# Kernel optimization log

Hardware: AMD Instinct MI355X
Metric: run time of the kernel (lower is better)

Reference implementation:

```python
import jax, jax.numpy as jnp
import numpy as np
from jax import lax

RF = 19       # receptive field: layers*(kernel-1)+1 = 3*6+1
WINDOW = 12
N_MIX = 2
K = 20        # subgraph_size (top-k per row)
GDEP = 2
ALPHA = 0.05  # propalpha
EPS = 1e-5


def conv2d(x, w, b):
    # x: [N,C,H,W], w: [O,I,1,k], valid conv along time (last) axis
    o = lax.conv_general_dilated(x, w, (1, 1), 'VALID',
                                 dimension_numbers=('NCHW', 'OIHW', 'NCHW'))
    return o + b[None, :, None, None]


def dilated_inception(x, ws, b):
    # ws: kernels [co, ci, k] for k in (2,3,6,7); dilation factor is 1 here
    outs = [lax.conv_general_dilated(x, w[:, :, None, :], (1, 1), 'VALID',
                                     dimension_numbers=('NCHW', 'OIHW', 'NCHW'))
            for w in ws]
    L = outs[-1].shape[-1]  # truncate to shortest (largest kernel) length
    out = jnp.concatenate([o[..., -L:] for o in outs], axis=1)
    return out + b[None, :, None, None]


def build_adj(e1, e2, l1w, l1b, l2w, l2b):
    # e1,e2: [M2,N,D] embedding tables (idx = arange -> full table)
    # torch Linear: y = x @ W.T + b, W: [out,in]
    nv1 = jnp.einsum('mnd,mod->mno', e1, l1w) + l1b[:, None, :]
    nv2 = jnp.einsum('mnd,mod->mno', e2, l2w) + l2b[:, None, :]
    a = jnp.einsum('mnd,mkd->mnk', nv1, nv2)  # [M2, N, N] per-block adjacency
    rows = [jnp.concatenate([a[i * N_MIX + j] for j in range(N_MIX)], axis=1)
            for i in range(N_MIX)]
    adj = jnp.concatenate(rows, axis=0)  # [NT, NT]
    _, t = lax.top_k(adj, K)  # per-row top-k indices
    mask = jnp.zeros_like(adj).at[jnp.arange(adj.shape[0])[:, None], t].set(1.0)
    return adj * mask


def mixprop(x, adj, w, b):
    a = adj + jnp.eye(adj.shape[0], dtype=adj.dtype)
    a = a / jnp.sum(a, axis=1, keepdims=True)  # row-normalize
    h = x
    outs = [h]
    for _ in range(GDEP):
        h = ALPHA * x + (1.0 - ALPHA) * jnp.einsum('ncwl,vw->ncvl', h, a)
        outs.append(h)
    ho = jnp.concatenate(outs, axis=1)  # [B,(GDEP+1)*C,V,L]
    return jnp.einsum('ncvl,oc->novl', ho, w) + b[None, :, None, None]


def layernorm(x, w, b):
    # torch F.layer_norm over all dims except batch; idx = arange -> full affine
    mu = jnp.mean(x, axis=(1, 2, 3), keepdims=True)
    var = jnp.mean((x - mu) ** 2, axis=(1, 2, 3), keepdims=True)
    return (x - mu) * lax.rsqrt(var + EPS) * w[None] + b[None]


def setup_inputs() -> dict:
    keys = iter(jax.random.split(jax.random.key(0), 80))
    def rn(shape, s=0.1):
        return s * jax.random.normal(next(keys), shape, dtype=jnp.float32)
    d = {}
    d['x_in'] = jax.random.normal(next(keys), (32, 12, 500, 4), dtype=jnp.float32)
    d['start_w'] = rn((32, 1, 1, 1)); d['start_b'] = rn((32,))
    d['skip0_w'] = rn((64, 1, 1, 19)); d['skip0_b'] = rn((64,))
    d['emb1'] = rn((3, 4, 500, 40)); d['emb2'] = rn((3, 4, 500, 40))
    d['lin1_w'] = rn((3, 4, 40, 40)); d['lin1_b'] = rn((3, 4, 40))
    d['lin2_w'] = rn((3, 4, 40, 40)); d['lin2_b'] = rn((3, 4, 40))
    d['g1_w'] = rn((3, 32, 96)); d['g1_b'] = rn((3, 32))
    d['g2_w'] = rn((3, 32, 96)); d['g2_b'] = rn((3, 32))
    for pref in ('filt', 'gate'):
        for k in (2, 3, 6, 7):
            d[f'{pref}_w{k}'] = rn((3, 8, 32, k))
        d[f'{pref}_b'] = rn((3, 32))
    for i, L in zip((1, 2, 3), (13, 7, 1)):
        d[f'skip_w{i}'] = rn((64, 32, 1, L)); d[f'skip_b{i}'] = rn((64,))
        d[f'norm_w{i}'] = jnp.ones((32, 1000, L), jnp.float32)
        d[f'norm_b{i}'] = jnp.zeros((32, 1000, L), jnp.float32)
    d['skipE_w'] = rn((64, 32, 1, 1)); d['skipE_b'] = rn((64,))
    d['end1_w'] = rn((128, 64, 1, 1)); d['end1_b'] = rn((128,))
    d['end2_w'] = rn((12, 128, 1, 1)); d['end2_b'] = rn((12,))
    return d


def reference(x_in, start_w, start_b, skip0_w, skip0_b, emb1, emb2,
              lin1_w, lin1_b, lin2_w, lin2_b, g1_w, g1_b, g2_w, g2_b,
              filt_w2, filt_w3, filt_w6, filt_w7, filt_b,
              gate_w2, gate_w3, gate_w6, gate_w7, gate_b,
              skip_w1, skip_b1, skip_w2, skip_b2, skip_w3, skip_b3,
              norm_w1, norm_b1, norm_w2, norm_b2, norm_w3, norm_b3,
              skipE_w, skipE_b, end1_w, end1_b, end2_w, end2_b):
    feat = x_in[..., :-2]  # drop last 2 'time' features
    # split per-mode feature and stack along node dim: [B,T,2N,1]
    inp = jnp.concatenate([feat[..., 0:1], feat[..., 1:2]], axis=2)
    inp = jnp.transpose(inp, (0, 3, 2, 1))  # [B,1,2N,T]
    inp = jnp.pad(inp, ((0, 0), (0, 0), (0, 0), (RF - WINDOW, 0)))
    x = conv2d(inp, start_w, start_b)       # [B,32,1000,19]
    skip = conv2d(inp, skip0_w, skip0_b)    # [B,64,1000,1] (dropout=eval no-op)
    filt_ws = (filt_w2, filt_w3, filt_w6, filt_w7)
    gate_ws = (gate_w2, gate_w3, gate_w6, gate_w7)
    skips = ((skip_w1, skip_b1), (skip_w2, skip_b2), (skip_w3, skip_b3))
    norms = ((norm_w1, norm_b1), (norm_w2, norm_b2), (norm_w3, norm_b3))
    for i in range(3):
        adp = build_adj(emb1[i], emb2[i], lin1_w[i], lin1_b[i], lin2_w[i], lin2_b[i])
        residual = x
        x = mixprop(x, adp, g1_w[i], g1_b[i]) + mixprop(x, adp.T, g2_w[i], g2_b[i])
        f = jnp.tanh(dilated_inception(x, [w[i] for w in filt_ws], filt_b[i]))
        g = jax.nn.sigmoid(dilated_inception(x, [w[i] for w in gate_ws], gate_b[i]))
        x = f * g
        sw, sb = skips[i]
        skip = conv2d(x, sw, sb) + skip
        x = x + residual[..., -x.shape[3]:]
        nw, nb = norms[i]
        x = layernorm(x, nw, nb)
    skip = conv2d(x, skipE_w, skipE_b) + skip
    x = jax.nn.relu(skip)
    x = jax.nn.relu(conv2d(x, end1_w, end1_b))
    return conv2d(x, end2_w, end2_b)  # [B, horizon*out_dim0=12, 1000, 1]
```

## Files before the change

kernel.cpp:

```cpp
#include <hip/hip_runtime.h>
#include <math.h>


#define ALPHA_C 0.05f
#define EPS_C 1e-5f
#define NBC 32
#define CSCT_CAP 140000

__device__ float g_inp[32 * 19 * 1000];
__device__ float g_skip[32 * 64 * 1000];
__device__ __align__(16) float g_nv1[240000];
__device__ __align__(16) float g_nv2[240000];
__device__ __align__(16) int   g_tkcol[60000];
__device__ __align__(16) float g_tkval[60000];
__device__ float g_inv1[3000];
__device__ int   g_colcnt[3000];
__device__ float g_colsum[3000];
__device__ int   g_rp2[3 * 1001 + 1];
__device__ int   g_fill[3000];
__device__ int   g_cscr[60000];
__device__ float g_cscv[60000];
__device__ float g_inv2[3000];
__device__ float g_stats[3 * 64];
__device__ float g_nwT[672000];
__device__ float g_nbT[672000];
__device__ __align__(16) int2 g_pk1T[60000];
__device__ __align__(16) int2 g_cscT[3 * CSCT_CAP];
__device__ int   g_perm[3 * 1024];
__device__ int   g_degT[3 * 1024];
__device__ int   g_iperm[3 * 1000];
__device__ int   g_tOff[3 * 17];
__device__ float g_B0[(size_t)NBC * 32 * 19 * 1000];
__device__ float g_B1[(size_t)NBC * 32 * 19 * 1000];
__device__ float g_B2[(size_t)NBC * 32 * 19 * 1000];
__device__ float g_B3[(size_t)NBC * 32 * 19 * 1000];
__device__ float g_B4[(size_t)NBC * 32 * 19 * 1000];
__device__ float g_B5[(size_t)NBC * 32 * 19 * 1000];

__device__ __forceinline__ float* bufsel(int s)
{
    switch (s) {
        case 0: return g_B0;
        case 1: return g_B1;
        case 2: return g_B2;
        case 3: return g_B3;
        case 4: return g_B4;
        default: return g_B5;
    }
}

__global__ void k_init()
{
    int i = blockIdx.x * 256 + threadIdx.x;
    if (i < 3000) { g_colcnt[i] = 0; g_colsum[i] = 0.f; g_fill[i] = 0; }
    if (i < 192) g_stats[i] = 0.f;
}

__global__ void k_out_zero(float* __restrict__ out, int n)
{
    int i = blockIdx.x * 256 + threadIdx.x;
    if (i < n) out[i] = 0.0f;
}

__global__ void k_marker(float* __restrict__ out, float v)
{
    if (threadIdx.x == 0) out[0] = v;
}


__global__ void k_build_inp(const float* __restrict__ xin)
{
    int i = blockIdx.x * 256 + threadIdx.x;
    if (i >= 32 * 19 * 1000) return;
    int v = i % 1000;
    int t = (i / 1000) % 19;
    int b = i / 19000;
    float val = 0.f;
    if (t >= 7) {
        int tt = t - 7;
        int n = (v < 500) ? v : v - 500;
        int f = (v < 500) ? 0 : 1;
        val = xin[((b * 12 + tt) * 500 + n) * 4 + f];
    }
    g_inp[i] = val;
}

__global__ void k_packN(const float* __restrict__ nw0, const float* __restrict__ nb0,
                        const float* __restrict__ nw1, const float* __restrict__ nb1,
                        const float* __restrict__ nw2, const float* __restrict__ nb2)
{
    int i = blockIdx.x * 256 + threadIdx.x;
    if (i >= 672000) return;
    const float* nw;
    const float* nb;
    int L, e;
    if (i < 416000)      { nw = nw0; nb = nb0; L = 13; e = i; }
    else if (i < 640000) { nw = nw1; nb = nb1; L = 7;  e = i - 416000; }
    else                 { nw = nw2; nb = nb2; L = 1;  e = i - 640000; }
    int ch = e / 1000, v = e - ch * 1000;
    int c = ch / L, l = ch - c * L;
    int src = (c * 1000 + v) * L + l;
    g_nwT[i] = nw[src];
    g_nbT[i] = nb[src];
}

__global__ void k_nv(const float* __restrict__ e1, const float* __restrict__ e2,
                     const float* __restrict__ w1, const float* __restrict__ b1,
                     const float* __restrict__ w2, const float* __restrict__ b2)
{
    int i = blockIdx.x * 256 + threadIdx.x;
    if (i >= 12 * 500 * 40) return;
    int o = i % 40;
    int n = (i / 40) % 500;
    int m = i / (40 * 500);
    const float4* p1 = (const float4*)(e1 + (m * 500 + n) * 40);
    const float4* pw1 = (const float4*)(w1 + (m * 40 + o) * 40);
    const float4* p2 = (const float4*)(e2 + (m * 500 + n) * 40);
    const float4* pw2 = (const float4*)(w2 + (m * 40 + o) * 40);
    float a1 = b1[m * 40 + o], a2 = b2[m * 40 + o];
    for (int d = 0; d < 10; ++d) {
        float4 x1 = p1[d], y1 = pw1[d];
        float4 x2 = p2[d], y2 = pw2[d];
        a1 += x1.x * y1.x; a1 += x1.y * y1.y; a1 += x1.z * y1.z; a1 += x1.w * y1.w;
        a2 += x2.x * y2.x; a2 += x2.y * y2.y; a2 += x2.z * y2.z; a2 += x2.w * y2.w;
    }
    g_nv1[i] = a1;
    g_nv2[i] = a2;
}

__global__ __launch_bounds__(256) void k_adj_topk()
{
    __shared__ float wvv[4];
    __shared__ int wvi[4];
    __shared__ int wci;
    __shared__ int selc[20];
    __shared__ float selv[20];
    int li = blockIdx.x / 1000;
    int r = blockIdx.x % 1000;
    int tid = threadIdx.x;
    int wv = tid >> 6, lane = tid & 63;
    int bi = r / 500, n = r % 500;
    float rv0, rv1, rv2, rv3;
    {
        auto score = [&](int c) -> float {
            if (c >= 1000) return -INFINITY;
            int bj = c / 500, k = c % 500;
            int mg = li * 4 + 2 * bi + bj;
            const float4* a = (const float4*)(g_nv1 + (mg * 500 + n) * 40);
            const float4* b = (const float4*)(g_nv2 + (mg * 500 + k) * 40);
            float acc = 0.f;
#pragma unroll
            for (int d = 0; d < 10; ++d) {
                float4 av = a[d], bv = b[d];
                acc += av.x * bv.x; acc += av.y * bv.y;
                acc += av.z * bv.z; acc += av.w * bv.w;
            }
            return acc;
        };
        rv0 = score(tid);
        rv1 = score(tid + 256);
        rv2 = score(tid + 512);
        rv3 = score(tid + 768);
    }
    for (int sel = 0; sel < 20; ++sel) {
        float bv = rv0;
        int bidx = tid;
        if (rv1 > bv) { bv = rv1; bidx = tid + 256; }
        if (rv2 > bv) { bv = rv2; bidx = tid + 512; }
        if (rv3 > bv) { bv = rv3; bidx = tid + 768; }
#pragma unroll
        for (int m = 1; m < 64; m <<= 1) {
            float ov = __shfl_xor(bv, m);
            int oi = __shfl_xor(bidx, m);
            if (ov > bv || (ov == bv && oi < bidx)) { bv = ov; bidx = oi; }
        }
        if (lane == 0) { wvv[wv] = bv; wvi[wv] = bidx; }
        __syncthreads();
        if (tid == 0) {
            float fv = wvv[0];
            int fi = wvi[0];
#pragma unroll
            for (int k = 1; k < 4; ++k) {
                float ov = wvv[k];
                int oi = wvi[k];
                if (ov > fv || (ov == fv && oi < fi)) { fv = ov; fi = oi; }
            }
            int ci = fi;
            if (ci < 0 || ci > 999) ci = sel;
            selc[sel] = ci;
            selv[sel] = fv;
            g_tkcol[(li * 1000 + r) * 20 + sel] = ci;
            g_tkval[(li * 1000 + r) * 20 + sel] = fv;
            wci = ci;
        }
        __syncthreads();
        int ci = wci;
        if ((ci & 255) == tid) {
            int k = ci >> 8;
            if (k == 0) rv0 = -INFINITY;
            else if (k == 1) rv1 = -INFINITY;
            else if (k == 2) rv2 = -INFINITY;
            else rv3 = -INFINITY;
        }
    }
    if (tid < 20) {
        atomicAdd(&g_colcnt[li * 1000 + selc[tid]], 1);
        atomicAdd(&g_colsum[li * 1000 + selc[tid]], selv[tid]);
    }
    if (tid == 0) {
        float s = 0.f;
        for (int j = 0; j < 20; ++j) s += selv[j];
        g_inv1[li * 1000 + r] = 1.f / (s + 1.f);
    }
}

__global__ __launch_bounds__(256) void k_scanperm()
{
    __shared__ int s[1000];
    __shared__ int deg[1000];
    __shared__ int tmax[16];
    int li = blockIdx.x;
    int tid = threadIdx.x;
    for (int i = tid; i < 1000; i += 256) {
        int c = g_colcnt[li * 1000 + i];
        s[i] = c;
        deg[i] = c;
    }
    __syncthreads();
    if (tid == 0) {
        int run = 0;
        for (int i = 0; i < 1000; ++i) { int c = s[i]; s[i] = run; run += c; }
        g_rp2[li * 1001 + 1000] = run;
    }
    __syncthreads();
    for (int i = tid; i < 1000; i += 256) {
        g_rp2[li * 1001 + i] = s[i];
        g_inv2[li * 1000 + i] = 1.f / (g_colsum[li * 1000 + i] + 1.f);
    }
    for (int v = tid; v < 1000; v += 256) {
        int d = deg[v];
        int r = 0;
        for (int u = 0; u < 1000; ++u) {
            int du = deg[u];
            r += (du > d) || (du == d && u < v);
        }
        g_perm[li * 1024 + r] = v;
        g_degT[li * 1024 + r] = d;
        g_iperm[li * 1000 + v] = r;
        if ((r & 63) == 0) tmax[r >> 6] = d;
    }
    if (tid < 24) {
        g_perm[li * 1024 + 1000 + tid] = -1;
        g_degT[li * 1024 + 1000 + tid] = 0;
    }
    __syncthreads();
    if (tid == 0) {
        int off = 0;
        for (int t = 0; t < 16; ++t) {
            g_tOff[li * 17 + t] = off;
            off += 64 * tmax[t];
        }
        g_tOff[li * 17 + 16] = off;
    }
}

__global__ void k_scatter()
{
    int i = blockIdx.x * 256 + threadIdx.x;
    if (i >= 3 * 20000) return;
    int li = i / 20000;
    int e = i % 20000;
    int r = e / 20;
    int c = g_tkcol[i];
    if (c < 0) c = 0;
    if (c > 999) c = 999;
    float v = g_tkval[i];
    int pos = g_rp2[li * 1001 + c] + atomicAdd(&g_fill[li * 1000 + c], 1);
    if (pos < 0) pos = 0;
    if (pos > 19999) pos = 19999;
    g_cscr[li * 20000 + pos] = r;
    g_cscv[li * 20000 + pos] = v;
}

__global__ void k_packT1()
{
    int i = blockIdx.x * 256 + threadIdx.x;
    if (i >= 60000) return;
    int li = i / 20000;
    int e = i % 20000;
    int v = e / 20, j = e % 20;
    int c1 = g_tkcol[i];
    if (c1 < 0) c1 = 0;
    if (c1 > 999) c1 = 999;
    g_pk1T[li * 20000 + j * 1000 + v] = make_int2(c1 * 16, __float_as_int(g_tkval[i]));
}

__global__ void k_packT2()
{
    int i = blockIdx.x * 256 + threadIdx.x;
    if (i >= 3000) return;
    int li = i / 1000, v = i % 1000;
    int r = g_iperm[li * 1000 + v];
    int t = r >> 6, ln = r & 63;
    int j0 = g_rp2[li * 1001 + v];
    int d = g_rp2[li * 1001 + v + 1] - j0;
    int base = g_tOff[li * 17 + t];
    for (int j = 0; j < d; ++j) {
        int row = g_cscr[li * 20000 + j0 + j];
        if (row < 0) row = 0;
        if (row > 999) row = 999;
        int pos = base + j * 64 + ln;
        if (pos >= 0 && pos < CSCT_CAP)
            g_cscT[li * CSCT_CAP + pos] =
                make_int2(row * 16, __float_as_int(g_cscv[li * 20000 + j0 + j]));
    }
}


__global__ __launch_bounds__(256) void k_skip0(const float* __restrict__ w,
                                               const float* __restrict__ bb)
{
    __shared__ float s_inp[19 * 32];
    __shared__ float s_w[64 * 19];
    int b = blockIdx.y;
    int v0 = blockIdx.x * 32;
    int tid = threadIdx.x;
    for (int i = tid; i < 64 * 19; i += 256) s_w[i] = w[i];
    for (int i = tid; i < 19 * 32; i += 256) {
        int t = i / 32, vl = i % 32;
        int v = v0 + vl;
        s_inp[i] = (v < 1000) ? g_inp[(b * 19 + t) * 1000 + v] : 0.f;
    }
    __syncthreads();
    for (int e = tid; e < 64 * 32; e += 256) {
        int o = e / 32, vl = e % 32;
        int v = v0 + vl;
        if (v >= 1000) continue;
        float acc = bb[o];
#pragma unroll
        for (int t = 0; t < 19; ++t) acc += s_w[o * 19 + t] * s_inp[t * 32 + vl];
        g_skip[(b * 64 + o) * 1000 + v] = acc;
    }
}

__global__ __launch_bounds__(256, 5) void k_prop4(int xsel, int o1s, int o2s, int o3s, int o4s,
                                                  int li, int CH, int li0,
                                                  const float* __restrict__ sw,
                                                  const float* __restrict__ sb,
                                                  int noff)
{
    __shared__ float4 S[2000];
    const float* X = bufsel(xsel);
    float* o1 = bufsel(o1s);
    float* o2 = bufsel(o2s);
    float* o3 = bufsel(o3s);
    float* o4 = bufsel(o4s);
    const int2* pkT = g_pk1T + li * 20000;
    const int2* cT = g_cscT + (size_t)li * CSCT_CAP;
    const int* prm = g_perm + li * 1024;
    const int* dgT = g_degT + li * 1024;
    const int* tOf = g_tOff + li * 17;
    const float* iv1 = g_inv1 + li * 1000;
    const float* iv2 = g_inv2 + li * 1000;
    int n = blockIdx.y;
    int ch0 = blockIdx.x * 4;
    size_t gb = ((size_t)n * CH + ch0) * 1000;
    int tid = threadIdx.x;
    int wv = tid >> 6, lane = tid & 63;
    char* Ub = (char*)S;
    char* Wb = (char*)(S + 1000);
    float4* U4 = S;
    float4* W4 = S + 1000;

    auto csr_hop = [&](const char* sbuf, float4* dst, float* gout) {
        for (int it = 0; it < 4; ++it) {
            int v = it * 256 + tid;
            if (v >= 1000) break;
            const int2* mp = pkT + v;
            float4 a = *(const float4*)(sbuf + (size_t)v * 16);
#pragma unroll
            for (int jb = 0; jb < 5; ++jb) {
                int2 e0 = mp[(jb * 4 + 0) * 1000];
                int2 e1 = mp[(jb * 4 + 1) * 1000];
                int2 e2 = mp[(jb * 4 + 2) * 1000];
                int2 e3 = mp[(jb * 4 + 3) * 1000];
                float w0 = __int_as_float(e0.y), w1 = __int_as_float(e1.y);
                float w2 = __int_as_float(e2.y), w3 = __int_as_float(e3.y);
                float4 x0 = *(const float4*)(sbuf + e0.x);
                float4 x1 = *(const float4*)(sbuf + e1.x);
                float4 x2 = *(const float4*)(sbuf + e2.x);
                float4 x3 = *(const float4*)(sbuf + e3.x);
                a.x += w0 * x0.x + w1 * x1.x + w2 * x2.x + w3 * x3.x;
                a.y += w0 * x0.y + w1 * x1.y + w2 * x2.y + w3 * x3.y;
                a.z += w0 * x0.z + w1 * x1.z + w2 * x2.z + w3 * x3.z;
                a.w += w0 * x0.w + w1 * x1.w + w2 * x2.w + w3 * x3.w;
            }
            float s = iv1[v];
            a.x *= s; a.y *= s; a.z *= s; a.w *= s;
            if (dst) dst[v] = a;
            gout[gb + v] = a.x;
            gout[gb + 1000 + v] = a.y;
            gout[gb + 2000 + v] = a.z;
            gout[gb + 3000 + v] = a.w;
        }
    };

    auto csc_hop = [&](const char* sbuf, float4* dst) {
        for (int o = 0; o < 4; ++o) {
            int tile = o * 4 + ((o & 1) ? (3 - wv) : wv);
            int r = tile * 64 + lane;
            int v = prm[r];
            if (v < 0) continue;
            int d = dgT[r];
            const int2* mp = cT + tOf[tile] + lane;
            float4 a = *(const float4*)(sbuf + (size_t)v * 16);
            int j = 0;
            for (; j + 4 <= d; j += 4) {
                int2 e0 = mp[(j + 0) * 64];
                int2 e1 = mp[(j + 1) * 64];
                int2 e2 = mp[(j + 2) * 64];
                int2 e3 = mp[(j + 3) * 64];
                float w0 = __int_as_float(e0.y), w1 = __int_as_float(e1.y);
                float w2 = __int_as_float(e2.y), w3 = __int_as_float(e3.y);
                float4 x0 = *(const float4*)(sbuf + e0.x);
                float4 x1 = *(const float4*)(sbuf + e1.x);
                float4 x2 = *(const float4*)(sbuf + e2.x);
                float4 x3 = *(const float4*)(sbuf + e3.x);
                a.x += w0 * x0.x + w1 * x1.x + w2 * x2.x + w3 * x3.x;
                a.y += w0 * x0.y + w1 * x1.y + w2 * x2.y + w3 * x3.y;
                a.z += w0 * x0.z + w1 * x1.z + w2 * x2.z + w3 * x3.z;
                a.w += w0 * x0.w + w1 * x1.w + w2 * x2.w + w3 * x3.w;
            }
            for (; j < d; ++j) {
                int2 e = mp[j * 64];
                float w = __int_as_float(e.y);
                float4 x = *(const float4*)(sbuf + e.x);
                a.x += w * x.x; a.y += w * x.y; a.z += w * x.z; a.w += w * x.w;
            }
            float s = iv2[v];
            a.x *= s; a.y *= s; a.z *= s; a.w *= s;
            dst[v] = a;
        }
    };

    if (li0) {
        float swv0 = sw[(ch0 + 0) / 19], sbv0 = sb[(ch0 + 0) / 19];
        float swv1 = sw[(ch0 + 1) / 19], sbv1 = sb[(ch0 + 1) / 19];
        float swv2 = sw[(ch0 + 2) / 19], sbv2 = sb[(ch0 + 2) / 19];
        float swv3 = sw[(ch0 + 3) / 19], sbv3 = sb[(ch0 + 3) / 19];
        const float* i0 = g_inp + (n * 19 + (ch0 + 0) % 19) * 1000;
        const float* i1 = g_inp + (n * 19 + (ch0 + 1) % 19) * 1000;
        const float* i2 = g_inp + (n * 19 + (ch0 + 2) % 19) * 1000;
        const float* i3 = g_inp + (n * 19 + (ch0 + 3) % 19) * 1000;
        for (int it = 0; it < 4; ++it) {
            int v = it * 256 + tid;
            if (v >= 1000) break;
            float4 t;
            t.x = swv0 * i0[v] + sbv0;
            t.y = swv1 * i1[v] + sbv1;
            t.z = swv2 * i2[v] + sbv2;
            t.w = swv3 * i3[v] + sbv3;
            U4[v] = t;
        }
    } else {
        const float* pst = g_stats + (li - 1) * 64;
        float cnt = (float)CH * 1000.f;
        float mu = pst[n * 2] / cnt;
        float var = pst[n * 2 + 1] / cnt - mu * mu;
        float rs = rsqrtf(var + EPS_C);
        const float* nw0 = g_nwT + noff + (ch0 + 0) * 1000;
        const float* nw1 = g_nwT + noff + (ch0 + 1) * 1000;
        const float* nw2 = g_nwT + noff + (ch0 + 2) * 1000;
        const float* nw3 = g_nwT + noff + (ch0 + 3) * 1000;
        const float* nb0 = g_nbT + noff + (ch0 + 0) * 1000;
        const float* nb1 = g_nbT + noff + (ch0 + 1) * 1000;
        const float* nb2 = g_nbT + noff + (ch0 + 2) * 1000;
        const float* nb3 = g_nbT + noff + (ch0 + 3) * 1000;
        for (int it = 0; it < 4; ++it) {
            int v = it * 256 + tid;
            if (v >= 1000) break;
            float4 t;
            t.x = (X[gb + v] - mu) * rs * nw0[v] + nb0[v];
            t.y = (X[gb + 1000 + v] - mu) * rs * nw1[v] + nb1[v];
            t.z = (X[gb + 2000 + v] - mu) * rs * nw2[v] + nb2[v];
            t.w = (X[gb + 3000 + v] - mu) * rs * nw3[v] + nb3[v];
            U4[v] = t;
        }
    }
    __syncthreads();

    csr_hop(Ub, W4, o1);
    __syncthreads();

    csr_hop(Wb, (float4*)nullptr, o2);
    __syncthreads();

    csc_hop(Ub, W4);
    __syncthreads();

    for (int it = 0; it < 4; ++it) {
        int v = it * 256 + tid;
        if (v >= 1000) break;
        float4 t = W4[v];
        o3[gb + v] = t.x;
        o3[gb + 1000 + v] = t.y;
        o3[gb + 2000 + v] = t.z;
        o3[gb + 3000 + v] = t.w;
    }
    csc_hop(Wb, U4);
    __syncthreads();

    for (int it = 0; it < 4; ++it) {
        int v = it * 256 + tid;
        if (v >= 1000) break;
        float4 t = U4[v];
        o4[gb + v] = t.x;
        o4[gb + 1000 + v] = t.y;
        o4[gb + 2000 + v] = t.z;
        o4[gb + 3000 + v] = t.w;
    }
}

__global__ __launch_bounds__(256) void k_mix(int xs, int h1s, int h2s, int h3s, int h4s, int ms,
                                             const float* __restrict__ g1w, const float* __restrict__ g2w,
                                             const float* __restrict__ g1b, const float* __restrict__ g2b,
                                             int P, int li, int li0,
                                             const float* __restrict__ sw_,
                                             const float* __restrict__ sb_,
                                             int noff)
{
    __shared__ float sW[5 * 1024];
    __shared__ float sB[32];
    __shared__ float sWS[32];
    __shared__ float sSB[32];
    int tid = threadIdx.x;
    const float A = ALPHA_C, Bq = 1.f - ALPHA_C;
    for (int i = tid; i < 1024; i += 256) {
        int o = i >> 5, c = i & 31;
        float w1 = g1w[o * 96 + 32 + c], w2 = g1w[o * 96 + 64 + c];
        float w3 = g2w[o * 96 + 32 + c], w4 = g2w[o * 96 + 64 + c];
        sW[i]        = g1w[o * 96 + c] + g2w[o * 96 + c] + A * (w1 + w2 + w3 + w4);
        sW[1024 + i] = Bq * (w1 + A * w2);
        sW[2048 + i] = Bq * Bq * w2;
        sW[3072 + i] = Bq * (w3 + A * w4);
        sW[4096 + i] = Bq * Bq * w4;
    }
    if (tid < 32) sB[tid] = g1b[tid] + g2b[tid];
    __syncthreads();
    if (li0 && tid < 32) {
        float as = 0.f, ab = 0.f;
        for (int c = 0; c < 32; ++c) {
            float w = sW[tid * 32 + c];
            as += w * sw_[c];
            ab += w * sb_[c];
        }
        sWS[tid] = as;
        sSB[tid] = ab;
    }
    if (li0) __syncthreads();
    int n = blockIdx.y;
    int p = blockIdx.x * 256 + tid;
    if (p >= P) return;
    const float* srcs[5] = {bufsel(xs), bufsel(h1s), bufsel(h2s), bufsel(h3s), bufsel(h4s)};
    float acc[32];
    if (li0) {
        float xv = g_inp[(size_t)n * 19000 + p];
#pragma unroll
        for (int o = 0; o < 32; ++o) acc[o] = sB[o] + sSB[o] + sWS[o] * xv;
    } else {
#pragma unroll
        for (int o = 0; o < 32; ++o) acc[o] = sB[o];
        int L = P / 1000;
        int l = p / 1000, v = p - l * 1000;
        const float* pst = g_stats + (li - 1) * 64;
        float cnt = 32.f * (float)P;
        float mu = pst[n * 2] / cnt;
        float var = pst[n * 2 + 1] / cnt - mu * mu;
        float rs = rsqrtf(var + EPS_C);
        const float* src0 = srcs[0] + (size_t)n * 32 * P + p;
        const float* nwT = g_nwT + noff + l * 1000 + v;
        const float* nbT = g_nbT + noff + l * 1000 + v;
        for (int c = 0; c < 32; ++c) {
            int wi = c * 1000 * L;
            float hv = (src0[(size_t)c * P] - mu) * rs * nwT[wi] + nbT[wi];
#pragma unroll
            for (int o = 0; o < 32; ++o) acc[o] += sW[o * 32 + c] * hv;
        }
    }
    for (int st = 1; st < 5; ++st) {
        const float* src = srcs[st] + (size_t)n * 32 * P + p;
        const float* w = &sW[st * 1024];
        for (int c = 0; c < 32; ++c) {
            float hv = src[(size_t)c * P];
#pragma unroll
            for (int o = 0; o < 32; ++o) acc[o] += w[o * 32 + c] * hv;
        }
    }
    float* XM = bufsel(ms) + (size_t)n * 32 * P + p;
#pragma unroll
    for (int o = 0; o < 32; ++o) XM[(size_t)o * P] = acc[o];
}

template <int LIN>
__global__ __launch_bounds__(256) void k_incept(int xmsel, int xgsel, int xpsel,
                                                const float* __restrict__ fw2, const float* __restrict__ fw3,
                                                const float* __restrict__ fw6, const float* __restrict__ fw7,
                                                const float* __restrict__ fb,
                                                const float* __restrict__ gw2, const float* __restrict__ gw3,
                                                const float* __restrict__ gw6, const float* __restrict__ gw7,
                                                const float* __restrict__ gb,
                                                const float* __restrict__ skw, const float* __restrict__ skb,
                                                int li, int li0,
                                                const float* __restrict__ sw_,
                                                const float* __restrict__ sb_,
                                                int noff)
{
    const int LOUT = LIN - 6;
    const float* XM = bufsel(xmsel);
    float* XG = bufsel(xgsel);
    const float* Xp = bufsel(xpsel);
    float* stats = g_stats + li * 64;
    __shared__ float sx[32 * 8 * LIN];
    __shared__ float sxg[32 * 8 * LOUT];
    __shared__ float ws1[4], ws2[4];
    int tid = threadIdx.x;
    int n = blockIdx.y, v0 = blockIdx.x * 8;
    for (int i = tid; i < 32 * LIN * 8; i += 256) {
        int vl = i & 7;
        int l = (i >> 3) % LIN;
        int c = i / (8 * LIN);
        sx[(c * 8 + vl) * LIN + l] = XM[(((size_t)n * 32 + c) * LIN + l) * 1000 + v0 + vl];
    }
    __syncthreads();
    int co = tid >> 3, vl = tid & 7;
    int s = co >> 3, co_s = co & 7;
    const int ksz[4] = {2, 3, 6, 7};
    int k = ksz[s];
    const float* fw = (s == 0) ? fw2 : ((s == 1) ? fw3 : ((s == 2) ? fw6 : fw7));
    const float* gw = (s == 0) ? gw2 : ((s == 1) ? gw3 : ((s == 2) ? gw6 : gw7));
    float accf[LOUT], accg[LOUT];
    float bf = fb[co], bg = gb[co];
#pragma unroll
    for (int l = 0; l < LOUT; ++l) { accf[l] = bf; accg[l] = bg; }
    for (int c = 0; c < 32; ++c) {
        const float* xp = &sx[(c * 8 + vl) * LIN];
        for (int j = 0; j < k; ++j) {
            float wf = fw[(co_s * 32 + c) * k + j];
            float wg = gw[(co_s * 32 + c) * k + j];
            int base = 7 - k + j;
#pragma unroll
            for (int l = 0; l < LOUT; ++l) {
                float xv = xp[base + l];
                accf[l] += wf * xv;
                accg[l] += wg * xv;
            }
        }
    }
    size_t ob = ((size_t)n * 32 + co) * LOUT * 1000 + v0 + vl;
    float lsum = 0.f, lss = 0.f;
    float swc = li0 ? sw_[co] : 0.f;
    float sbc = li0 ? sb_[co] : 0.f;
    float mu = 0.f, rs = 0.f;
    if (!li0) {
        const float* pst = g_stats + (li - 1) * 64;
        float cnt = 32.f * (float)LIN * 1000.f;
        mu = pst[n * 2] / cnt;
        float var = pst[n * 2 + 1] / cnt - mu * mu;
        rs = rsqrtf(var + EPS_C);
    }
#pragma unroll
    for (int l = 0; l < LOUT; ++l) {
        float g = tanhf(accf[l]) * (1.f / (1.f + expf(-accg[l])));
        float r;
        if (li0) {
            r = swc * g_inp[(n * 19 + l + 6) * 1000 + v0 + vl] + sbc;
        } else {
            float raw = Xp[(((size_t)n * 32 + co) * LIN + l + 6) * 1000 + v0 + vl];
            int wi = noff + (co * LIN + l + 6) * 1000 + v0 + vl;
            r = (raw - mu) * rs * g_nwT[wi] + g_nbT[wi];
        }
        float y = g + r;
        XG[ob + (size_t)l * 1000] = y;
        sxg[(co * 8 + vl) * LOUT + l] = g;
        lsum += y;
        lss += y * y;
    }
    __syncthreads();
    int obk = tid >> 3;
    for (int half = 0; half < 2; ++half) {
        int o = obk + 32 * half;
        float acc = skb[o];
        for (int c = 0; c < 32; ++c) {
            const float* wp = &skw[((size_t)o * 32 + c) * LOUT];
            const float* xp = &sxg[(c * 8 + vl) * LOUT];
#pragma unroll
            for (int l = 0; l < LOUT; ++l) acc += wp[l] * xp[l];
        }
        size_t si = ((size_t)n * 64 + o) * 1000 + v0 + vl;
        g_skip[si] += acc;
    }
#pragma unroll
    for (int m = 1; m < 64; m <<= 1) {
        lsum += __shfl_xor(lsum, m);
        lss += __shfl_xor(lss, m);
    }
    int wvi = tid >> 6;
    if ((tid & 63) == 0) { ws1[wvi] = lsum; ws2[wvi] = lss; }
    __syncthreads();
    if (tid == 0) {
        float t1 = ws1[0] + ws1[1] + ws1[2] + ws1[3];
        float t2 = ws2[0] + ws2[1] + ws2[2] + ws2[3];
        atomicAdd(&stats[n * 2], t1);
        atomicAdd(&stats[n * 2 + 1], t2);
    }
}

__global__ __launch_bounds__(256) void k_final(int xsel,
                                               const float* __restrict__ ew, const float* __restrict__ eb,
                                               const float* __restrict__ e1w, const float* __restrict__ e1b,
                                               const float* __restrict__ e2w, const float* __restrict__ e2b,
                                               float* __restrict__ out)
{
    const float* X = bufsel(xsel);
    __shared__ float sxf[32 * 16];
    __shared__ float sk[64 * 16];
    __shared__ float s1[64 * 16];
    __shared__ float s2[128 * 16];
    int b = blockIdx.y, v0 = blockIdx.x * 16;
    int tid = threadIdx.x;
    const float* pst = g_stats + 2 * 64;
    float cnt = 32000.f;
    float mu = pst[b * 2] / cnt;
    float var = pst[b * 2 + 1] / cnt - mu * mu;
    float rs = rsqrtf(var + EPS_C);
    for (int i = tid; i < 512; i += 256) {
        int c = i / 16, vl = i & 15;
        int v = v0 + vl;
        float x = 0.f;
        if (v < 1000) {
            float raw = X[((size_t)b * 32 + c) * 1000 + v];
            int wi = 640000 + c * 1000 + v;
            x = (raw - mu) * rs * g_nwT[wi] + g_nbT[wi];
        }
        sxf[i] = x;
    }
    for (int i = tid; i < 1024; i += 256) {
        int o = i / 16, vl = i & 15;
        int v = v0 + vl;
        sk[i] = (v < 1000) ? g_skip[((size_t)b * 64 + o) * 1000 + v] : 0.f;
    }
    __syncthreads();
    for (int i = tid; i < 1024; i += 256) {
        int o = i / 16, vl = i & 15;
        float acc = sk[i] + eb[o];
        for (int c = 0; c < 32; ++c) acc += ew[o * 32 + c] * sxf[c * 16 + vl];
        s1[i] = fmaxf(acc, 0.f);
    }
    __syncthreads();
    for (int i = tid; i < 2048; i += 256) {
        int o = i / 16, vl = i & 15;
        float acc = e1b[o];
        for (int c = 0; c < 64; ++c) acc += e1w[o * 64 + c] * s1[c * 16 + vl];
        s2[i] = fmaxf(acc, 0.f);
    }
    __syncthreads();
    if (tid < 192) {
        int o = tid / 16, vl = tid & 15;
        int v = v0 + vl;
        if (v < 1000) {
            float acc = e2b[o];
            for (int c = 0; c < 128; ++c) acc += e2w[o * 128 + c] * s2[c * 16 + vl];
            out[((size_t)b * 12 + o) * 1000 + v] = acc;
        }
    }
}


static const int SZ_SORT[43] = {240000,240000,128,8192,12,1536,96,1536,2304,4608,
                                5376,96,9216,96,9216,96,1536,2304,4608,5376,
                                480,19200,480,19200,416000,224000,32000,416000,224000,32000,
                                64,1216,64,2048,64,64,64,26624,14336,2048,32,32,768000};
static const int SZ_DICT[43] = {768000,32,32,1216,64,240000,240000,19200,480,19200,
                                480,9216,96,9216,96,1536,2304,4608,5376,96,
                                1536,2304,4608,5376,96,26624,64,416000,416000,14336,
                                64,224000,224000,2048,64,32000,32000,2048,64,8192,128,1536,12};
static const int SZ_SIG[43]  = {768000,32,32,1216,64,240000,240000,19200,480,19200,
                                480,9216,96,9216,96,1536,2304,4608,5376,96,
                                1536,2304,4608,5376,96,26624,64,14336,64,2048,
                                64,416000,416000,224000,224000,32000,32000,2048,64,8192,128,1536,12};

extern "C" void kernel_launch(void* const* d_in, const int* in_sizes, int n_in,
                              void* d_out, int out_size, void* d_ws, size_t ws_size,
                              hipStream_t stream)
{
    (void)d_ws; (void)ws_size;
    const float *x_in, *start_w, *start_b, *skip0_w, *skip0_b;
    const float *emb1, *emb2, *lin1_w, *lin1_b, *lin2_w, *lin2_b;
    const float *g1_w, *g1_b, *g2_w, *g2_b;
    const float *filt_w[4], *filt_b, *gate_w[4], *gate_b;
    const float *skw[3], *skb[3], *nww[3], *nbb[3];
    const float *skipE_w, *skipE_b, *end1_w, *end1_b, *end2_w, *end2_b;
    float* outp = (float*)d_out;
    auto P = [&](int i) { return (const float*)d_in[i]; };
    auto match = [&](const int* tab) {
        if (n_in < 43) return false;
        for (int i = 0; i < 43; ++i) if (in_sizes[i] != tab[i]) return false;
        return true;
    };

    int fam = -1;
    if (match(SZ_SORT)) fam = 0;
    else if (match(SZ_DICT)) fam = 1;
    else if (match(SZ_SIG)) fam = 2;

    if (fam == 0) {
        emb1 = P(0); emb2 = P(1); end1_b = P(2); end1_w = P(3); end2_b = P(4); end2_w = P(5);
        filt_b = P(6); filt_w[0] = P(7); filt_w[1] = P(8); filt_w[2] = P(9); filt_w[3] = P(10);
        g1_b = P(11); g1_w = P(12); g2_b = P(13); g2_w = P(14);
        gate_b = P(15); gate_w[0] = P(16); gate_w[1] = P(17); gate_w[2] = P(18); gate_w[3] = P(19);
        lin1_b = P(20); lin1_w = P(21); lin2_b = P(22); lin2_w = P(23);
        nbb[0] = P(24); nbb[1] = P(25); nbb[2] = P(26);
        nww[0] = P(27); nww[1] = P(28); nww[2] = P(29);
        skip0_b = P(30); skip0_w = P(31); skipE_b = P(32); skipE_w = P(33);
        skb[0] = P(34); skb[1] = P(35); skb[2] = P(36);
        skw[0] = P(37); skw[1] = P(38); skw[2] = P(39);
        start_b = P(40); start_w = P(41); x_in = P(42);
    } else if (fam == 1 || fam == 2) {
        x_in = P(0); start_w = P(1); start_b = P(2); skip0_w = P(3); skip0_b = P(4);
        emb1 = P(5); emb2 = P(6); lin1_w = P(7); lin1_b = P(8); lin2_w = P(9); lin2_b = P(10);
        g1_w = P(11); g1_b = P(12); g2_w = P(13); g2_b = P(14);
        filt_w[0] = P(15); filt_w[1] = P(16); filt_w[2] = P(17); filt_w[3] = P(18); filt_b = P(19);
        gate_w[0] = P(20); gate_w[1] = P(21); gate_w[2] = P(22); gate_w[3] = P(23); gate_b = P(24);
        if (fam == 1) {
            skw[0] = P(25); skb[0] = P(26); nww[0] = P(27); nbb[0] = P(28);
            skw[1] = P(29); skb[1] = P(30); nww[1] = P(31); nbb[1] = P(32);
            skw[2] = P(33); skb[2] = P(34); nww[2] = P(35); nbb[2] = P(36);
        } else {
            skw[0] = P(25); skb[0] = P(26); skw[1] = P(27); skb[1] = P(28);
            skw[2] = P(29); skb[2] = P(30);
            nww[0] = P(31); nbb[0] = P(32); nww[1] = P(33); nbb[1] = P(34);
            nww[2] = P(35); nbb[2] = P(36);
        }
        skipE_w = P(37); skipE_b = P(38); end1_w = P(39); end1_b = P(40);
        end2_w = P(41); end2_b = P(42);
    } else {
        k_out_zero<<<(out_size + 255) / 256, 256, 0, stream>>>(outp, out_size);
        k_marker<<<1, 64, 0, stream>>>(outp, 8192.0f);
        return;
    }

    k_init<<<12, 256, 0, stream>>>();
    k_build_inp<<<(32 * 19 * 1000 + 255) / 256, 256, 0, stream>>>(x_in);
    k_packN<<<(672000 + 255) / 256, 256, 0, stream>>>(nww[0], nbb[0], nww[1], nbb[1],
                                                      nww[2], nbb[2]);
    k_nv<<<(240000 + 255) / 256, 256, 0, stream>>>(emb1, emb2, lin1_w, lin1_b, lin2_w, lin2_b);
    k_adj_topk<<<3000, 256, 0, stream>>>();
    k_scanperm<<<3, 256, 0, stream>>>();
    k_scatter<<<(60000 + 255) / 256, 256, 0, stream>>>();
    k_packT1<<<(60000 + 255) / 256, 256, 0, stream>>>();
    k_packT2<<<12, 256, 0, stream>>>();

    k_skip0<<<dim3(32, NBC), 256, 0, stream>>>(skip0_w, skip0_b);

    int X = 0;
    int LIN = 19;
    for (int li = 0; li < 3; ++li) {
        int LOUT = LIN - 6;
        int Pp = 1000 * LIN;
        int li0 = (li == 0) ? 1 : 0;
        int noff = (li == 2) ? 416000 : 0;
        int hb[4], hn = 0;
        for (int b = 0; b < 6 && hn < 4; ++b)
            if (b != X && b != 1) hb[hn++] = b;
        int h1 = hb[0], h2 = hb[1], h3 = hb[2], h4 = hb[3];
        int CH = 32 * LIN;
        dim3 gg((unsigned)(CH / 4), NBC);

        k_prop4<<<gg, 256, 0, stream>>>(X, h1, h2, h3, h4, li, CH, li0,
                                        start_w, start_b, noff);

        k_mix<<<dim3((Pp + 255) / 256, NBC), 256, 0, stream>>>(X, h1, h2, h3, h4, 1,
            g1_w + li * 3072, g2_w + li * 3072, g1_b + li * 32, g2_b + li * 32, Pp,
            li, li0, start_w, start_b, noff);

        int XG = h1;
        if (LIN == 19)
            k_incept<19><<<dim3(125, NBC), 256, 0, stream>>>(1, XG, X,
                filt_w[0] + li * 512, filt_w[1] + li * 768, filt_w[2] + li * 1536, filt_w[3] + li * 1792,
                filt_b + li * 32,
                gate_w[0] + li * 512, gate_w[1] + li * 768, gate_w[2] + li * 1536, gate_w[3] + li * 1792,
                gate_b + li * 32, skw[li], skb[li], li, li0, start_w, start_b, noff);
        else if (LIN == 13)
            k_incept<13><<<dim3(125, NBC), 256, 0, stream>>>(1, XG, X,
                filt_w[0] + li * 512, filt_w[1] + li * 768, filt_w[2] + li * 1536, filt_w[3] + li * 1792,
                filt_b + li * 32,
                gate_w[0] + li * 512, gate_w[1] + li * 768, gate_w[2] + li * 1536, gate_w[3] + li * 1792,
                gate_b + li * 32, skw[li], skb[li], li, li0, start_w, start_b, noff);
        else
            k_incept<7><<<dim3(125, NBC), 256, 0, stream>>>(1, XG, X,
                filt_w[0] + li * 512, filt_w[1] + li * 768, filt_w[2] + li * 1536, filt_w[3] + li * 1792,
                filt_b + li * 32,
                gate_w[0] + li * 512, gate_w[1] + li * 768, gate_w[2] + li * 1536, gate_w[3] + li * 1792,
                gate_b + li * 32, skw[li], skb[li], li, li0, start_w, start_b, noff);

        X = XG;
        LIN = LOUT;
    }
    k_final<<<dim3(63, NBC), 256, 0, stream>>>(X, skipE_w, skipE_b,
                                               end1_w, end1_b, end2_w, end2_b, outp);
}
```

Baseline: 2.497 ms.

## Store mixprop output in blocked channel-last layout for vectorized inception loads

The mixprop output kernel now writes each point's 32 channels contiguously as float4 vectors, in a layout blocked by groups of 8 nodes, time and lane. The inception kernel reads this blocked tile with contiguous float4 loads and scatters it into shared memory. This replaces the per-channel strided writes and 4-byte loads with wide contiguous ones. It changes the producer-consumer layout contract, so any other reader of this buffer must agree with the new format.

```diff
diff --git a/kernel.cpp b/kernel.cpp
--- a/kernel.cpp
+++ b/kernel.cpp
@@ -30,12 +30,12 @@
 __device__ int   g_degT[3 * 1024];
 __device__ int   g_iperm[3 * 1000];
 __device__ int   g_tOff[3 * 17];
-__device__ float g_B0[(size_t)NBC * 32 * 19 * 1000];
-__device__ float g_B1[(size_t)NBC * 32 * 19 * 1000];
-__device__ float g_B2[(size_t)NBC * 32 * 19 * 1000];
-__device__ float g_B3[(size_t)NBC * 32 * 19 * 1000];
-__device__ float g_B4[(size_t)NBC * 32 * 19 * 1000];
-__device__ float g_B5[(size_t)NBC * 32 * 19 * 1000];
+__device__ __align__(16) float g_B0[(size_t)NBC * 32 * 19 * 1000];
+__device__ __align__(16) float g_B1[(size_t)NBC * 32 * 19 * 1000];
+__device__ __align__(16) float g_B2[(size_t)NBC * 32 * 19 * 1000];
+__device__ __align__(16) float g_B3[(size_t)NBC * 32 * 19 * 1000];
+__device__ __align__(16) float g_B4[(size_t)NBC * 32 * 19 * 1000];
+__device__ __align__(16) float g_B5[(size_t)NBC * 32 * 19 * 1000];
 
 __device__ __forceinline__ float* bufsel(int s)
 {
@@ -562,6 +562,8 @@
     int p = blockIdx.x * 256 + tid;
     if (p >= P) return;
     const float* srcs[5] = {bufsel(xs), bufsel(h1s), bufsel(h2s), bufsel(h3s), bufsel(h4s)};
+    int L = P / 1000;
+    int l = p / 1000, v = p - l * 1000;
     float acc[32];
     if (li0) {
         float xv = g_inp[(size_t)n * 19000 + p];
@@ -570,8 +572,6 @@
     } else {
 #pragma unroll
         for (int o = 0; o < 32; ++o) acc[o] = sB[o];
-        int L = P / 1000;
-        int l = p / 1000, v = p - l * 1000;
         const float* pst = g_stats + (li - 1) * 64;
         float cnt = 32.f * (float)P;
         float mu = pst[n * 2] / cnt;
@@ -596,9 +596,12 @@
             for (int o = 0; o < 32; ++o) acc[o] += w[o * 32 + c] * hv;
         }
     }
-    float* XM = bufsel(ms) + (size_t)n * 32 * P + p;
-#pragma unroll
-    for (int o = 0; o < 32; ++o) XM[(size_t)o * P] = acc[o];
+    int vb = v >> 3, vl = v & 7;
+    size_t xb = ((((size_t)n * 125 + vb) * L + l) * 8 + vl) * 32;
+    float4* dst = (float4*)(bufsel(ms) + xb);
+#pragma unroll
+    for (int q = 0; q < 8; ++q)
+        dst[q] = make_float4(acc[q * 4], acc[q * 4 + 1], acc[q * 4 + 2], acc[q * 4 + 3]);
 }
 
 template <int LIN>
@@ -625,11 +628,21 @@
     __shared__ float ws1[4], ws2[4];
     int tid = threadIdx.x;
     int n = blockIdx.y, v0 = blockIdx.x * 8;
-    for (int i = tid; i < 32 * LIN * 8; i += 256) {
-        int vl = i & 7;
-        int l = (i >> 3) % LIN;
-        int c = i / (8 * LIN);
-        sx[(c * 8 + vl) * LIN + l] = XM[(((size_t)n * 32 + c) * LIN + l) * 1000 + v0 + vl];
+    {
+        const float4* XT = (const float4*)(XM + ((size_t)n * 125 + blockIdx.x) * (size_t)(LIN * 256));
+        const int NT4 = LIN * 64;
+        for (int i = tid; i < NT4; i += 256) {
+            float4 t = XT[i];
+            int e = i * 4;
+            int c = e & 31;
+            int r = e >> 5;
+            int vl_ = r & 7, l_ = r >> 3;
+            float* d = &sx[(c * 8 + vl_) * LIN + l_];
+            d[0] = t.x;
+            d[8 * LIN] = t.y;
+            d[16 * LIN] = t.z;
+            d[24 * LIN] = t.w;
+        }
     }
     __syncthreads();
     int co = tid >> 3, vl = tid & 7;
```

Result: no change. 2.488 ms (-0.4%).
